# Optimization experiments

Hardware: AMD Instinct MI355X
Metric: run time of the kernel (lower is better)

The kernel has to match this reference:

```python
import jax, jax.numpy as jnp
import numpy as np

B, C, H, W = 8, 128, 128, 128
HEADS = 8

def setup_inputs() -> dict:
    key = jax.random.key(0)
    k1, k2 = jax.random.split(key)
    x1 = jax.random.normal(k1, (B, C, H, W), dtype=jnp.float32)
    x2 = jax.random.normal(k2, (B, C, H, W), dtype=jnp.float32)
    return {"x1": x1, "x2": x2}

def reference(x1, x2):
    b, c, h, w = x1.shape
    n = h * w
    hk = c // HEADS  # head key channels
    hv = c // HEADS  # head value channels
    # [B,C,N] layouts (channels-first, as in torch after transpose back)
    vals = x1.reshape(b, c, n)   # values come from x1
    kq = x2.reshape(b, c, n)     # keys and queries come from x2
    k = kq.reshape(b, HEADS, hk, n)
    v = vals.reshape(b, HEADS, hv, n)
    key_sm = jax.nn.softmax(k, axis=-1)   # softmax over N (torch dim=2)
    query_sm = jax.nn.softmax(k, axis=2)  # softmax over head channels (torch dim=1)
    # context = key @ value^T : [B,h,hk,hv]
    context = jnp.einsum('bhkn,bhvn->bhkv', key_sm, v)
    # attended = context^T @ query : [B,h,hv,N]
    attended = jnp.einsum('bhkv,bhkn->bhvn', context, query_sm)
    return attended.reshape(b, c, H, W)
```

## Files before the change

kernel.cpp:

```cpp
#include <hip/hip_runtime.h>
#include <math.h>

#define N_     16384
#define N4     4096
#define BHN    64
#define CH     16
#define CHUNKS 32

#define WS_PART 0
#define WS_ZP   (BHN * CHUNKS * 256)

typedef __attribute__((ext_vector_type(8))) short short8;
typedef __attribute__((ext_vector_type(4))) float f32x4;

static __device__ __forceinline__ short f2bf(float f) {
    __bf16 b = (__bf16)f;
    return __builtin_bit_cast(short, b);
}

__global__ __launch_bounds__(256) void k_ctx_mfma(const float* __restrict__ x1,
                                                  const float* __restrict__ x2,
                                                  float* __restrict__ ws) {
    int chunk = blockIdx.x;
    int bh    = blockIdx.y;
    int tid   = threadIdx.x;
    int w = tid >> 6, l = tid & 63;

    __shared__ __align__(16) short e_s[16][520];
    __shared__ __align__(16) short v_s[16][520];
    __shared__ float cred[4][256];
    __shared__ float zs[16];

    {
        const float* src = (w < 2) ? x2 : x1;
        int r0 = (w & 1) * 8;
        const float* base = src + (size_t)(bh * CH + r0) * N_ + chunk * 512;

        float4 A[16];
        #pragma unroll
        for (int i = 0; i < 8; ++i) {
            const float4* p = (const float4*)(base + (size_t)i * N_);
            A[2 * i]     = p[2 * l];
            A[2 * i + 1] = p[2 * l + 1];
        }

        if (w < 2) {
            #pragma unroll
            for (int i = 0; i < 8; ++i) {
                float4 a = A[2 * i], b = A[2 * i + 1];
                float e0 = __expf(a.x), e1 = __expf(a.y), e2 = __expf(a.z), e3 = __expf(a.w);
                float e4 = __expf(b.x), e5 = __expf(b.y), e6 = __expf(b.z), e7 = __expf(b.w);
                float z = ((e0 + e1) + (e2 + e3)) + ((e4 + e5) + (e6 + e7));
                #pragma unroll
                for (int off = 1; off < 64; off <<= 1) z += __shfl_xor(z, off);
                if (l == 0) zs[r0 + i] = z;
                short8 pk = {f2bf(e0), f2bf(e1), f2bf(e2), f2bf(e3),
                             f2bf(e4), f2bf(e5), f2bf(e6), f2bf(e7)};
                *(short8*)&e_s[r0 + i][l * 8] = pk;
            }
        } else {
            #pragma unroll
            for (int i = 0; i < 8; ++i) {
                float4 a = A[2 * i], b = A[2 * i + 1];
                short8 pv = {f2bf(a.x), f2bf(a.y), f2bf(a.z), f2bf(a.w),
                             f2bf(b.x), f2bf(b.y), f2bf(b.z), f2bf(b.w)};
                *(short8*)&v_s[r0 + i][l * 8] = pv;
            }
        }
    }
    __syncthreads();

    int row16 = l & 15;
    int q     = l >> 4;
    f32x4 acc = {0.f, 0.f, 0.f, 0.f};
    #pragma unroll
    for (int s = 0; s < 4; ++s) {
        int col = w * 128 + s * 32 + q * 8;
        short8 af = *(const short8*)&e_s[row16][col];
        short8 bv = *(const short8*)&v_s[row16][col];
        acc = __builtin_amdgcn_mfma_f32_16x16x32_bf16(af, bv, acc, 0, 0, 0);
    }

    #pragma unroll
    for (int r = 0; r < 4; ++r)
        cred[w][(q * 4 + r) * 16 + row16] = acc[r];
    __syncthreads();

    if (tid < 16)
        ws[WS_ZP + (bh * CHUNKS + chunk) * 16 + tid] = zs[tid];
    float c = (cred[0][tid] + cred[1][tid]) + (cred[2][tid] + cred[3][tid]);
    ws[WS_PART + (size_t)(bh * CHUNKS + chunk) * 256 + tid] = c;
}

__global__ __launch_bounds__(256) void k_attend(const float* __restrict__ x2,
                                                const float* __restrict__ ws,
                                                float* __restrict__ out) {
    int cb  = blockIdx.x;
    int bh  = blockIdx.y;
    int tid = threadIdx.x;

    __shared__ float q_s[16][256];
    __shared__ float ctxs[256];
    __shared__ float rzs[16];

    float csum = 0.f;
    #pragma unroll
    for (int c = 0; c < CHUNKS; ++c)
        csum += ws[WS_PART + (size_t)(bh * CHUNKS + c) * 256 + tid];
    if (tid < 16) {
        float z = 0.f;
        #pragma unroll
        for (int c = 0; c < CHUNKS; ++c)
            z += ws[WS_ZP + (bh * CHUNKS + c) * 16 + tid];
        rzs[tid] = 1.0f / z;
    }

    const float4* px = (const float4*)(x2 + (size_t)bh * CH * N_);
    int base4 = cb * 64;
    #pragma unroll
    for (int r = 0; r < 4; ++r) {
        int idx = r * 256 + tid;
        int ch = idx >> 6, j = idx & 63;
        float4 v = px[(size_t)ch * N4 + base4 + j];
        *(float4*)&q_s[ch][j * 4] = v;
    }
    __syncthreads();

    ctxs[tid] = csum * rzs[tid >> 4];

    {
        int col = tid;
        float kv[16];
        #pragma unroll
        for (int c = 0; c < 16; ++c) kv[c] = q_s[c][col];
        float mx = kv[0];
        #pragma unroll
        for (int c = 1; c < 16; ++c) mx = fmaxf(mx, kv[c]);
        float s = 0.f;
        #pragma unroll
        for (int c = 0; c < 16; ++c) { kv[c] = __expf(kv[c] - mx); s += kv[c]; }
        float rs = 1.0f / s;
        #pragma unroll
        for (int c = 0; c < 16; ++c) q_s[c][col] = kv[c] * rs;
    }
    __syncthreads();

    int vg = tid >> 6, cq = tid & 63;
    int vv0 = vg * 4, c0 = cq * 4;
    float4 a0 = make_float4(0.f,0.f,0.f,0.f);
    float4 a1 = a0, a2 = a0, a3 = a0;
    #pragma unroll
    for (int kk = 0; kk < 16; ++kk) {
        float4 cx = *(const float4*)&ctxs[kk * 16 + vv0];
        float4 q4 = *(const float4*)&q_s[kk][c0];
        a0.x = fmaf(q4.x, cx.x, a0.x); a0.y = fmaf(q4.x, cx.y, a0.y);
        a0.z = fmaf(q4.x, cx.z, a0.z); a0.w = fmaf(q4.x, cx.w, a0.w);
        a1.x = fmaf(q4.y, cx.x, a1.x); a1.y = fmaf(q4.y, cx.y, a1.y);
        a1.z = fmaf(q4.y, cx.z, a1.z); a1.w = fmaf(q4.y, cx.w, a1.w);
        a2.x = fmaf(q4.z, cx.x, a2.x); a2.y = fmaf(q4.z, cx.y, a2.y);
        a2.z = fmaf(q4.z, cx.z, a2.z); a2.w = fmaf(q4.z, cx.w, a2.w);
        a3.x = fmaf(q4.w, cx.x, a3.x); a3.y = fmaf(q4.w, cx.y, a3.y);
        a3.z = fmaf(q4.w, cx.z, a3.z); a3.w = fmaf(q4.w, cx.w, a3.w);
    }
    size_t outbase = (size_t)bh * CH * N_ + (size_t)cb * 256 + c0;
    float4 o;
    o = make_float4(a0.x, a1.x, a2.x, a3.x);
    *(float4*)&out[outbase + (size_t)(vv0 + 0) * N_] = o;
    o = make_float4(a0.y, a1.y, a2.y, a3.y);
    *(float4*)&out[outbase + (size_t)(vv0 + 1) * N_] = o;
    o = make_float4(a0.z, a1.z, a2.z, a3.z);
    *(float4*)&out[outbase + (size_t)(vv0 + 2) * N_] = o;
    o = make_float4(a0.w, a1.w, a2.w, a3.w);
    *(float4*)&out[outbase + (size_t)(vv0 + 3) * N_] = o;
}

extern "C" void kernel_launch(void* const* d_in, const int* in_sizes, int n_in,
                              void* d_out, int out_size, void* d_ws, size_t ws_size,
                              hipStream_t stream) {
    const float* x1 = (const float*)d_in[0];
    const float* x2 = (const float*)d_in[1];
    float* out = (float*)d_out;
    float* ws  = (float*)d_ws;

    k_ctx_mfma <<<dim3(CHUNKS, BHN), 256, 0, stream>>>(x1, x2, ws);
    k_attend   <<<dim3(64, BHN),     256, 0, stream>>>(x2, ws, out);
}
```

Measured before the change: 58.14 us.

## Split key exp/bf16 conversion into a row-wise prep kernel before MFMA context

Adds a prep kernel that computes exp(key) and the full softmax denominator per row, converting keys and values to bf16 in a workspace. The context kernel then loads the half-size bf16 data with smaller chunks (64 per head), and the attend kernel reads the finished row sums instead of reducing per-chunk partials. The aim is a row-level z reduction and more parallelism in the context stage. The cost is an extra launch and an extra round trip of bf16 intermediates through global memory. The old two-kernel path stays as a fallback when the workspace is too small.

```diff
diff --git a/kernel.cpp b/kernel.cpp
--- a/kernel.cpp
+++ b/kernel.cpp
@@ -5,10 +5,8 @@
 #define N4     4096
 #define BHN    64
 #define CH     16
-#define CHUNKS 32
-
-#define WS_PART 0
-#define WS_ZP   (BHN * CHUNKS * 256)
+#define ROWS   1024
+#define CHUNKS 64
 
 typedef __attribute__((ext_vector_type(8))) short short8;
 typedef __attribute__((ext_vector_type(4))) float f32x4;
@@ -18,55 +16,86 @@
     return __builtin_bit_cast(short, b);
 }
 
-__global__ __launch_bounds__(256) void k_ctx_mfma(const float* __restrict__ x1,
-                                                  const float* __restrict__ x2,
-                                                  float* __restrict__ ws) {
+#define WS_NEED ((size_t)ROWS * N_ * 2 * 2 + ROWS * 4 + (size_t)BHN * CHUNKS * 256 * 4)
+
+__global__ __launch_bounds__(256) void k_prep(const float* __restrict__ x1,
+                                              const float* __restrict__ x2,
+                                              short* __restrict__ e_bf,
+                                              short* __restrict__ v_bf,
+                                              float* __restrict__ z) {
+    int row = blockIdx.x;
+    int tid = threadIdx.x;
+    int w = tid >> 6, l = tid & 63;
+
+    __shared__ float zred[4];
+
+    {
+        const float4* p = (const float4*)(x2 + (size_t)row * N_);
+        short8* q = (short8*)(e_bf + (size_t)row * N_);
+        float zacc = 0.f;
+        #pragma unroll
+        for (int it = 0; it < 4; ++it) {
+            int i0 = it * 1024 + 2 * tid;
+            int i1 = i0 + 512;
+            float4 a0 = p[i0], a1 = p[i0 + 1];
+            float4 b0 = p[i1], b1 = p[i1 + 1];
+            float e0=__expf(a0.x), e1=__expf(a0.y), e2=__expf(a0.z), e3=__expf(a0.w);
+            float e4=__expf(a1.x), e5=__expf(a1.y), e6=__expf(a1.z), e7=__expf(a1.w);
+            float f0=__expf(b0.x), f1=__expf(b0.y), f2=__expf(b0.z), f3=__expf(b0.w);
+            float f4=__expf(b1.x), f5=__expf(b1.y), f6=__expf(b1.z), f7=__expf(b1.w);
+            zacc += (((e0+e1)+(e2+e3)) + ((e4+e5)+(e6+e7)))
+                  + (((f0+f1)+(f2+f3)) + ((f4+f5)+(f6+f7)));
+            short8 s0 = {f2bf(e0),f2bf(e1),f2bf(e2),f2bf(e3),
+                         f2bf(e4),f2bf(e5),f2bf(e6),f2bf(e7)};
+            short8 s1 = {f2bf(f0),f2bf(f1),f2bf(f2),f2bf(f3),
+                         f2bf(f4),f2bf(f5),f2bf(f6),f2bf(f7)};
+            q[i0 >> 1] = s0;
+            q[i1 >> 1] = s1;
+        }
+        #pragma unroll
+        for (int off = 1; off < 64; off <<= 1) zacc += __shfl_xor(zacc, off);
+        if (l == 0) zred[w] = zacc;
+    }
+    {
+        const float4* p = (const float4*)(x1 + (size_t)row * N_);
+        short8* q = (short8*)(v_bf + (size_t)row * N_);
+        #pragma unroll
+        for (int it = 0; it < 4; ++it) {
+            int i0 = it * 1024 + 2 * tid;
+            int i1 = i0 + 512;
+            float4 a0 = p[i0], a1 = p[i0 + 1];
+            float4 b0 = p[i1], b1 = p[i1 + 1];
+            short8 s0 = {f2bf(a0.x),f2bf(a0.y),f2bf(a0.z),f2bf(a0.w),
+                         f2bf(a1.x),f2bf(a1.y),f2bf(a1.z),f2bf(a1.w)};
+            short8 s1 = {f2bf(b0.x),f2bf(b0.y),f2bf(b0.z),f2bf(b0.w),
+                         f2bf(b1.x),f2bf(b1.y),f2bf(b1.z),f2bf(b1.w)};
+            q[i0 >> 1] = s0;
+            q[i1 >> 1] = s1;
+        }
+    }
+    __syncthreads();
+    if (tid == 0) z[row] = (zred[0] + zred[1]) + (zred[2] + zred[3]);
+}
+
+__global__ __launch_bounds__(256) void k_ctx(const short* __restrict__ e_bf,
+                                             const short* __restrict__ v_bf,
+                                             float* __restrict__ part) {
     int chunk = blockIdx.x;
     int bh    = blockIdx.y;
     int tid   = threadIdx.x;
     int w = tid >> 6, l = tid & 63;
 
-    __shared__ __align__(16) short e_s[16][520];
-    __shared__ __align__(16) short v_s[16][520];
+    __shared__ __align__(16) short es[16 * 264];
+    __shared__ __align__(16) short vs[16 * 264];
     __shared__ float cred[4][256];
-    __shared__ float zs[16];
-
-    {
-        const float* src = (w < 2) ? x2 : x1;
-        int r0 = (w & 1) * 8;
-        const float* base = src + (size_t)(bh * CH + r0) * N_ + chunk * 512;
-
-        float4 A[16];
-        #pragma unroll
-        for (int i = 0; i < 8; ++i) {
-            const float4* p = (const float4*)(base + (size_t)i * N_);
-            A[2 * i]     = p[2 * l];
-            A[2 * i + 1] = p[2 * l + 1];
-        }
-
-        if (w < 2) {
-            #pragma unroll
-            for (int i = 0; i < 8; ++i) {
-                float4 a = A[2 * i], b = A[2 * i + 1];
-                float e0 = __expf(a.x), e1 = __expf(a.y), e2 = __expf(a.z), e3 = __expf(a.w);
-                float e4 = __expf(b.x), e5 = __expf(b.y), e6 = __expf(b.z), e7 = __expf(b.w);
-                float z = ((e0 + e1) + (e2 + e3)) + ((e4 + e5) + (e6 + e7));
-                #pragma unroll
-                for (int off = 1; off < 64; off <<= 1) z += __shfl_xor(z, off);
-                if (l == 0) zs[r0 + i] = z;
-                short8 pk = {f2bf(e0), f2bf(e1), f2bf(e2), f2bf(e3),
-                             f2bf(e4), f2bf(e5), f2bf(e6), f2bf(e7)};
-                *(short8*)&e_s[r0 + i][l * 8] = pk;
-            }
-        } else {
-            #pragma unroll
-            for (int i = 0; i < 8; ++i) {
-                float4 a = A[2 * i], b = A[2 * i + 1];
-                short8 pv = {f2bf(a.x), f2bf(a.y), f2bf(a.z), f2bf(a.w),
-                             f2bf(b.x), f2bf(b.y), f2bf(b.z), f2bf(b.w)};
-                *(short8*)&v_s[r0 + i][l * 8] = pv;
-            }
-        }
+
+    #pragma unroll
+    for (int p = 0; p < 2; ++p) {
+        int idx = p * 256 + tid;
+        int row = idx >> 5, grp = idx & 31;
+        size_t g = (size_t)(bh * CH + row) * N_ + chunk * 256 + grp * 8;
+        *(short8*)&es[row * 264 + grp * 8] = *(const short8*)(e_bf + g);
+        *(short8*)&vs[row * 264 + grp * 8] = *(const short8*)(v_bf + g);
     }
     __syncthreads();
 
@@ -74,10 +103,10 @@
     int q     = l >> 4;
     f32x4 acc = {0.f, 0.f, 0.f, 0.f};
     #pragma unroll
-    for (int s = 0; s < 4; ++s) {
-        int col = w * 128 + s * 32 + q * 8;
-        short8 af = *(const short8*)&e_s[row16][col];
-        short8 bv = *(const short8*)&v_s[row16][col];
+    for (int s = 0; s < 2; ++s) {
+        int col = w * 64 + s * 32 + q * 8;
+        short8 af = *(const short8*)&es[row16 * 264 + col];
+        short8 bv = *(const short8*)&vs[row16 * 264 + col];
         acc = __builtin_amdgcn_mfma_f32_16x16x32_bf16(af, bv, acc, 0, 0, 0);
     }
 
@@ -86,14 +115,13 @@
         cred[w][(q * 4 + r) * 16 + row16] = acc[r];
     __syncthreads();
 
-    if (tid < 16)
-        ws[WS_ZP + (bh * CHUNKS + chunk) * 16 + tid] = zs[tid];
     float c = (cred[0][tid] + cred[1][tid]) + (cred[2][tid] + cred[3][tid]);
-    ws[WS_PART + (size_t)(bh * CHUNKS + chunk) * 256 + tid] = c;
+    part[(size_t)(bh * CHUNKS + chunk) * 256 + tid] = c;
 }
 
 __global__ __launch_bounds__(256) void k_attend(const float* __restrict__ x2,
-                                                const float* __restrict__ ws,
+                                                const float* __restrict__ part,
+                                                const float* __restrict__ z,
                                                 float* __restrict__ out) {
     int cb  = blockIdx.x;
     int bh  = blockIdx.y;
@@ -106,14 +134,8 @@
     float csum = 0.f;
     #pragma unroll
     for (int c = 0; c < CHUNKS; ++c)
-        csum += ws[WS_PART + (size_t)(bh * CHUNKS + c) * 256 + tid];
-    if (tid < 16) {
-        float z = 0.f;
-        #pragma unroll
-        for (int c = 0; c < CHUNKS; ++c)
-            z += ws[WS_ZP + (bh * CHUNKS + c) * 16 + tid];
-        rzs[tid] = 1.0f / z;
-    }
+        csum += part[(size_t)(bh * CHUNKS + c) * 256 + tid];
+    if (tid < 16) rzs[tid] = 1.0f / z[bh * CH + tid];
 
     const float4* px = (const float4*)(x2 + (size_t)bh * CH * N_);
     int base4 = cb * 64;
@@ -174,14 +196,166 @@
     *(float4*)&out[outbase + (size_t)(vv0 + 3) * N_] = o;
 }
 
+#define FCHUNKS 32
+#define FWS_PART 0
+#define FWS_ZP   (BHN * FCHUNKS * 256)
+
+__global__ __launch_bounds__(256) void k_ctx_fb(const float* __restrict__ x1,
+                                                const float* __restrict__ x2,
+                                                float* __restrict__ ws) {
+    int chunk = blockIdx.x, bh = blockIdx.y;
+    int tid = threadIdx.x;
+    int w = tid >> 6, l = tid & 63;
+    __shared__ __align__(16) short e_s[16][520];
+    __shared__ __align__(16) short v_s[16][520];
+    __shared__ float cred[4][256];
+    __shared__ float zs[16];
+    {
+        const float* src = (w < 2) ? x2 : x1;
+        int r0 = (w & 1) * 8;
+        const float* base = src + (size_t)(bh * CH + r0) * N_ + chunk * 512;
+        float4 A[16];
+        #pragma unroll
+        for (int i = 0; i < 8; ++i) {
+            const float4* p = (const float4*)(base + (size_t)i * N_);
+            A[2 * i] = p[2 * l]; A[2 * i + 1] = p[2 * l + 1];
+        }
+        if (w < 2) {
+            #pragma unroll
+            for (int i = 0; i < 8; ++i) {
+                float4 a = A[2 * i], b = A[2 * i + 1];
+                float e0=__expf(a.x), e1=__expf(a.y), e2=__expf(a.z), e3=__expf(a.w);
+                float e4=__expf(b.x), e5=__expf(b.y), e6=__expf(b.z), e7=__expf(b.w);
+                float zz = ((e0+e1)+(e2+e3)) + ((e4+e5)+(e6+e7));
+                #pragma unroll
+                for (int off = 1; off < 64; off <<= 1) zz += __shfl_xor(zz, off);
+                if (l == 0) zs[r0 + i] = zz;
+                short8 pk = {f2bf(e0),f2bf(e1),f2bf(e2),f2bf(e3),
+                             f2bf(e4),f2bf(e5),f2bf(e6),f2bf(e7)};
+                *(short8*)&e_s[r0 + i][l * 8] = pk;
+            }
+        } else {
+            #pragma unroll
+            for (int i = 0; i < 8; ++i) {
+                float4 a = A[2 * i], b = A[2 * i + 1];
+                short8 pv = {f2bf(a.x),f2bf(a.y),f2bf(a.z),f2bf(a.w),
+                             f2bf(b.x),f2bf(b.y),f2bf(b.z),f2bf(b.w)};
+                *(short8*)&v_s[r0 + i][l * 8] = pv;
+            }
+        }
+    }
+    __syncthreads();
+    int row16 = l & 15, q = l >> 4;
+    f32x4 acc = {0.f, 0.f, 0.f, 0.f};
+    #pragma unroll
+    for (int s = 0; s < 4; ++s) {
+        int col = w * 128 + s * 32 + q * 8;
+        short8 af = *(const short8*)&e_s[row16][col];
+        short8 bv = *(const short8*)&v_s[row16][col];
+        acc = __builtin_amdgcn_mfma_f32_16x16x32_bf16(af, bv, acc, 0, 0, 0);
+    }
+    #pragma unroll
+    for (int r = 0; r < 4; ++r)
+        cred[w][(q * 4 + r) * 16 + row16] = acc[r];
+    __syncthreads();
+    if (tid < 16) ws[FWS_ZP + (bh * FCHUNKS + chunk) * 16 + tid] = zs[tid];
+    float c = (cred[0][tid] + cred[1][tid]) + (cred[2][tid] + cred[3][tid]);
+    ws[FWS_PART + (size_t)(bh * FCHUNKS + chunk) * 256 + tid] = c;
+}
+
+__global__ __launch_bounds__(256) void k_attend_fb(const float* __restrict__ x2,
+                                                   const float* __restrict__ ws,
+                                                   float* __restrict__ out) {
+    int cb = blockIdx.x, bh = blockIdx.y;
+    int tid = threadIdx.x;
+    __shared__ float q_s[16][256];
+    __shared__ float ctxs[256];
+    __shared__ float rzs[16];
+    float csum = 0.f;
+    #pragma unroll
+    for (int c = 0; c < FCHUNKS; ++c)
+        csum += ws[FWS_PART + (size_t)(bh * FCHUNKS + c) * 256 + tid];
+    if (tid < 16) {
+        float z = 0.f;
+        #pragma unroll
+        for (int c = 0; c < FCHUNKS; ++c)
+            z += ws[FWS_ZP + (bh * FCHUNKS + c) * 16 + tid];
+        rzs[tid] = 1.0f / z;
+    }
+    const float4* px = (const float4*)(x2 + (size_t)bh * CH * N_);
+    int base4 = cb * 64;
+    #pragma unroll
+    for (int r = 0; r < 4; ++r) {
+        int idx = r * 256 + tid;
+        int ch = idx >> 6, j = idx & 63;
+        float4 v = px[(size_t)ch * N4 + base4 + j];
+        *(float4*)&q_s[ch][j * 4] = v;
+    }
+    __syncthreads();
+    ctxs[tid] = csum * rzs[tid >> 4];
+    {
+        int col = tid;
+        float kv[16];
+        #pragma unroll
+        for (int c = 0; c < 16; ++c) kv[c] = q_s[c][col];
+        float mx = kv[0];
+        #pragma unroll
+        for (int c = 1; c < 16; ++c) mx = fmaxf(mx, kv[c]);
+        float s = 0.f;
+        #pragma unroll
+        for (int c = 0; c < 16; ++c) { kv[c] = __expf(kv[c] - mx); s += kv[c]; }
+        float rs = 1.0f / s;
+        #pragma unroll
+        for (int c = 0; c < 16; ++c) q_s[c][col] = kv[c] * rs;
+    }
+    __syncthreads();
+    int vg = tid >> 6, cq = tid & 63;
+    int vv0 = vg * 4, c0 = cq * 4;
+    float4 a0 = make_float4(0.f,0.f,0.f,0.f);
+    float4 a1 = a0, a2 = a0, a3 = a0;
+    #pragma unroll
+    for (int kk = 0; kk < 16; ++kk) {
+        float4 cx = *(const float4*)&ctxs[kk * 16 + vv0];
+        float4 q4 = *(const float4*)&q_s[kk][c0];
+        a0.x = fmaf(q4.x, cx.x, a0.x); a0.y = fmaf(q4.x, cx.y, a0.y);
+        a0.z = fmaf(q4.x, cx.z, a0.z); a0.w = fmaf(q4.x, cx.w, a0.w);
+        a1.x = fmaf(q4.y, cx.x, a1.x); a1.y = fmaf(q4.y, cx.y, a1.y);
+        a1.z = fmaf(q4.y, cx.z, a1.z); a1.w = fmaf(q4.y, cx.w, a1.w);
+        a2.x = fmaf(q4.z, cx.x, a2.x); a2.y = fmaf(q4.z, cx.y, a2.y);
+        a2.z = fmaf(q4.z, cx.z, a2.z); a2.w = fmaf(q4.z, cx.w, a2.w);
+        a3.x = fmaf(q4.w, cx.x, a3.x); a3.y = fmaf(q4.w, cx.y, a3.y);
+        a3.z = fmaf(q4.w, cx.z, a3.z); a3.w = fmaf(q4.w, cx.w, a3.w);
+    }
+    size_t outbase = (size_t)bh * CH * N_ + (size_t)cb * 256 + c0;
+    float4 o;
+    o = make_float4(a0.x, a1.x, a2.x, a3.x);
+    *(float4*)&out[outbase + (size_t)(vv0 + 0) * N_] = o;
+    o = make_float4(a0.y, a1.y, a2.y, a3.y);
+    *(float4*)&out[outbase + (size_t)(vv0 + 1) * N_] = o;
+    o = make_float4(a0.z, a1.z, a2.z, a3.z);
+    *(float4*)&out[outbase + (size_t)(vv0 + 2) * N_] = o;
+    o = make_float4(a0.w, a1.w, a2.w, a3.w);
+    *(float4*)&out[outbase + (size_t)(vv0 + 3) * N_] = o;
+}
+
 extern "C" void kernel_launch(void* const* d_in, const int* in_sizes, int n_in,
                               void* d_out, int out_size, void* d_ws, size_t ws_size,
                               hipStream_t stream) {
     const float* x1 = (const float*)d_in[0];
     const float* x2 = (const float*)d_in[1];
     float* out = (float*)d_out;
-    float* ws  = (float*)d_ws;
-
-    k_ctx_mfma <<<dim3(CHUNKS, BHN), 256, 0, stream>>>(x1, x2, ws);
-    k_attend   <<<dim3(64, BHN),     256, 0, stream>>>(x2, ws, out);
-}
+
+    if (ws_size >= WS_NEED) {
+        short* e_bf = (short*)d_ws;
+        short* v_bf = e_bf + (size_t)ROWS * N_;
+        float* z    = (float*)(v_bf + (size_t)ROWS * N_);
+        float* part = z + ROWS;
+        k_prep  <<<ROWS,             256, 0, stream>>>(x1, x2, e_bf, v_bf, z);
+        k_ctx   <<<dim3(CHUNKS, BHN), 256, 0, stream>>>(e_bf, v_bf, part);
+        k_attend<<<dim3(64, BHN),    256, 0, stream>>>(x2, part, z, out);
+    } else {
+        float* ws = (float*)d_ws;
+        k_ctx_fb   <<<dim3(FCHUNKS, BHN), 256, 0, stream>>>(x1, x2, ws);
+        k_attend_fb<<<dim3(64, BHN),      256, 0, stream>>>(x2, ws, out);
+    }
+}
```

After: 76.14 us. +30.9%, slower.
